# Kernel optimization log

Measured on AMD Instinct MI355X. Metric: run time of the kernel, lower is better.

Reference implementation:

```python
import jax, jax.numpy as jnp
import numpy as np

H = 8          # num_heads
BM = 128       # block_size_m
BN = 128       # block_size_n
EPS = 1e-6
CAUSAL = True  # config.causal


def setup_inputs() -> dict:
    key = jax.random.key(0)
    ks = jax.random.split(key, 5)
    B, N, D = 1, 2048, 512
    s = 1.0 / np.sqrt(D)
    # small-scale x so projected points mostly stay inside the Poincare ball
    x = jax.random.normal(ks[0], (B, N, D), jnp.float32) * 0.05
    return {
        'x': x,
        'c': jnp.ones((1,), jnp.float32),
        'Wq': jax.random.normal(ks[1], (D, D), jnp.float32) * s,
        'bq': jnp.zeros((D,), jnp.float32),
        'Wk': jax.random.normal(ks[2], (D, D), jnp.float32) * s,
        'bk': jnp.zeros((D,), jnp.float32),
        'Wv': jax.random.normal(ks[3], (D, D), jnp.float32) * s,
        'bv': jnp.zeros((D,), jnp.float32),
        'Wo': jax.random.normal(ks[4], (D, D), jnp.float32) * s,
        'bo': jnp.zeros((D,), jnp.float32),
    }


def reference(x, c, Wq, bq, Wk, bk, Wv, bv, Wo, bo):
    B, N, D = x.shape
    Dh = D // H
    cc = jnp.clip(jnp.abs(c), 1e-6)            # (1,) learned curvature, abs+clamp as in torch
    sqrt_c = jnp.sqrt(jnp.clip(cc, EPS))

    def proj(W, b):
        return (x @ W + b).reshape(B, N, H, Dh).transpose(0, 2, 1, 3)  # (B,H,N,Dh)

    q, k, v = proj(Wq, bq), proj(Wk, bk), proj(Wv, bv)

    # Poincare distance: ||q-k||^2 expanded via norms (same math as explicit diff tensor)
    qn = (q ** 2).sum(-1)                      # (B,H,N)
    kn = (k ** 2).sum(-1)                      # (B,H,N)
    qk = jnp.einsum('bhmd,bhnd->bhmn', q, k)   # (B,H,N,N)
    diff_sq = jnp.clip(qn[..., :, None] + kn[..., None, :] - 2.0 * qk, 0.0)
    denom = jnp.clip((1.0 - cc * qn)[..., :, None] * (1.0 - cc * kn)[..., None, :], EPS)
    arg = jnp.clip(1.0 + 2.0 * cc * diff_sq / denom, 1.0 + EPS)
    scores = -jnp.arccosh(arg) / sqrt_c        # (B,H,N,N)

    # block-wise softmax: each 128x128 block subtracts ITS OWN max (faithful to torch code,
    # which omits cross-block max rescaling), then exp-sums are accumulated across blocks.
    nbm, nbn = N // BM, N // BN
    s = scores.reshape(B, H, nbm, BM, nbn, BN)
    row = jnp.arange(nbm)[:, None]
    col = jnp.arange(nbn)[None, :]
    skip = (col > row) if CAUSAL else jnp.zeros((nbm, nbn), bool)   # skipped upper blocks
    diag = (col == row) if CAUSAL else jnp.zeros((nbm, nbn), bool)
    tri = jnp.triu(jnp.ones((BM, BN), bool), 1)
    mask = skip[:, None, :, None] | (diag[:, None, :, None] & tri[None, :, None, :])  # (nbm,BM,nbn,BN)

    s_masked = jnp.where(mask, -jnp.inf, s)
    bmax = s_masked.max(axis=-1, keepdims=True)                      # per-block-row max over BN
    bmax = jnp.where(jnp.isfinite(bmax), bmax, 0.0)                  # skipped blocks -> safe
    e = jnp.where(mask, 0.0, jnp.exp(s - bmax))                      # (B,H,nbm,BM,nbn,BN)

    normalizer = jnp.clip(e.sum(axis=(4, 5)).reshape(B, H, N), EPS)  # (B,H,N)
    vb = v.reshape(B, H, nbn, BN, Dh)
    out = jnp.einsum('bhrmcn,bhcnd->bhrmd', e, vb).reshape(B, H, N, Dh)
    out = out / normalizer[..., None]
    out = out.transpose(0, 2, 1, 3).reshape(B, N, D)
    return out @ Wo + bo
```

## Files before the change

kernel.cpp:

```cpp
#include <hip/hip_runtime.h>
#include <math.h>

#define D_MODEL 512
#define NHEADS  8
#define NSEQ    2048
#define NBLK    16
#define NCHUNK  72
#define EPSF    1e-6f
#define WPLANE  262144

typedef _Float16 v8h __attribute__((ext_vector_type(8)));
typedef _Float16 v4h __attribute__((ext_vector_type(4)));
typedef float    v4f __attribute__((ext_vector_type(4)));

static __device__ __forceinline__ v4f mfma16h(v8h a, v8h b, v4f c) {
  return __builtin_amdgcn_mfma_f32_16x16x32_f16(a, b, c, 0, 0, 0);
}

__global__ __launch_bounds__(256) void prep_wx(const float* __restrict__ W0,
                                               const float* __restrict__ W1,
                                               const float* __restrict__ W2,
                                               const float* __restrict__ W3,
                                               const float* __restrict__ x,
                                               _Float16* __restrict__ Wth,
                                               _Float16* __restrict__ xh) {
  const int z = blockIdx.z;
  const int tid = threadIdx.x;
  if (z == 4) {
    const int wg = blockIdx.y * 8 + blockIdx.x;
    int base = wg * 4096 + tid;
#pragma unroll
    for (int l = 0; l < 16; ++l) {
      int idx = base + l * 256;
      float4 v = reinterpret_cast<const float4*>(x)[idx];
      v4h o;
      o[0] = (_Float16)v.x; o[1] = (_Float16)v.y;
      o[2] = (_Float16)v.z; o[3] = (_Float16)v.w;
      reinterpret_cast<v4h*>(xh)[idx] = o;
    }
    return;
  }
  __shared__ float T[64][68];
  const float* W = (z == 0) ? W0 : (z == 1) ? W1 : (z == 2) ? W2 : W3;
  const int kb = blockIdx.x * 64;
  const int nb = blockIdx.y * 64;
#pragma unroll
  for (int l = 0; l < 4; ++l) {
    int f = tid + l * 256;
    int row = f >> 4, c4 = f & 15;
    float4 v = *reinterpret_cast<const float4*>(&W[(size_t)(kb + row) * D_MODEL + nb + c4 * 4]);
    T[c4 * 4 + 0][row] = v.x; T[c4 * 4 + 1][row] = v.y;
    T[c4 * 4 + 2][row] = v.z; T[c4 * 4 + 3][row] = v.w;
  }
  __syncthreads();
  _Float16* oh = Wth + (size_t)z * WPLANE;
#pragma unroll
  for (int l = 0; l < 4; ++l) {
    int f = tid + l * 256;
    int n_ = f >> 4, k4 = f & 15;
    v4h h4;
    h4[0] = (_Float16)T[n_][k4 * 4 + 0];
    h4[1] = (_Float16)T[n_][k4 * 4 + 1];
    h4[2] = (_Float16)T[n_][k4 * 4 + 2];
    h4[3] = (_Float16)T[n_][k4 * 4 + 3];
    *reinterpret_cast<v4h*>(&oh[(size_t)(nb + n_) * D_MODEL + kb + k4 * 4]) = h4;
  }
}

__global__ __launch_bounds__(256) void qkv_gemm(
    const _Float16* __restrict__ xh, const _Float16* __restrict__ Wth,
    const float* __restrict__ bq, const float* __restrict__ bk,
    const float* __restrict__ bv,
    _Float16* __restrict__ Qp, _Float16* __restrict__ Kp,
    _Float16* __restrict__ Vtb,
    float* __restrict__ Qn_, float* __restrict__ Kn_) {
  __shared__ _Float16 Ah[64][72];
  __shared__ _Float16 Bh[64][72];
  __shared__ float npar[2][64];
  const int z = blockIdx.z;
  const _Float16* Bt = Wth + (size_t)z * WPLANE;
  const float* bias = (z == 0) ? bq : (z == 1) ? bk : bv;
  _Float16* outp = (z == 0) ? Qp : Kp;

  const int bx = blockIdx.x, by = blockIdx.y;
  const int tid = threadIdx.x;
  const int wid = tid >> 6, lane = tid & 63;
  const int wr = wid >> 1, wc = wid & 1;
  const int g = lane >> 4, lx = lane & 15;

  v4f acc[2][2];
#pragma unroll
  for (int i = 0; i < 2; ++i)
#pragma unroll
    for (int j = 0; j < 2; ++j) acc[i][j] = v4f{0.f, 0.f, 0.f, 0.f};

  for (int k0 = 0; k0 < 8; ++k0) {
    __syncthreads();
#pragma unroll
    for (int l = 0; l < 2; ++l) {
      int f = tid + l * 256;
      int row = f >> 3, c8 = f & 7;
      *reinterpret_cast<uint4*>(&Ah[row][c8 * 8]) =
          *reinterpret_cast<const uint4*>(&xh[(size_t)(by * 64 + row) * D_MODEL + k0 * 64 + c8 * 8]);
      *reinterpret_cast<uint4*>(&Bh[row][c8 * 8]) =
          *reinterpret_cast<const uint4*>(&Bt[(size_t)(bx * 64 + row) * D_MODEL + k0 * 64 + c8 * 8]);
    }
    __syncthreads();
    v8h a[2][2], b[2][2];
#pragma unroll
    for (int i = 0; i < 2; ++i)
#pragma unroll
      for (int ks = 0; ks < 2; ++ks) {
        a[i][ks] = *reinterpret_cast<const v8h*>(&Ah[wr * 32 + i * 16 + lx][ks * 32 + g * 8]);
        b[i][ks] = *reinterpret_cast<const v8h*>(&Bh[wc * 32 + i * 16 + lx][ks * 32 + g * 8]);
      }
#pragma unroll
    for (int i = 0; i < 2; ++i)
#pragma unroll
      for (int j = 0; j < 2; ++j) {
        acc[i][j] = mfma16h(a[i][0], b[j][0], acc[i][j]);
        acc[i][j] = mfma16h(a[i][1], b[j][1], acc[i][j]);
      }
  }

  if (z < 2) {
    float np[2][4];
#pragma unroll
    for (int i = 0; i < 2; ++i)
#pragma unroll
      for (int r = 0; r < 4; ++r) np[i][r] = 0.f;
#pragma unroll
    for (int j = 0; j < 2; ++j) {
      const int col = bx * 64 + wc * 32 + j * 16 + lx;
      const float bj = bias[col];
#pragma unroll
      for (int i = 0; i < 2; ++i)
#pragma unroll
        for (int r = 0; r < 4; ++r) {
          const int row = by * 64 + wr * 32 + i * 16 + g * 4 + r;
          float v = acc[i][j][r] + bj;
          _Float16 hv = (_Float16)v;
          outp[(size_t)row * D_MODEL + col] = hv;
          float vr = (float)hv;
          np[i][r] = fmaf(vr, vr, np[i][r]);
        }
    }
#pragma unroll
    for (int i = 0; i < 2; ++i)
#pragma unroll
      for (int r = 0; r < 4; ++r) {
        float s = np[i][r];
        s += __shfl_xor(s, 1, 64);
        s += __shfl_xor(s, 2, 64);
        s += __shfl_xor(s, 4, 64);
        s += __shfl_xor(s, 8, 64);
        if (lx == 0) npar[wc][wr * 32 + i * 16 + g * 4 + r] = s;
      }
    __syncthreads();
    if (tid < 64) {
      float s = npar[0][tid] + npar[1][tid];
      float* Nout = (z == 0) ? Qn_ : Kn_;
      Nout[bx * NSEQ + by * 64 + tid] = s;
    }
  } else {
    __syncthreads();
    _Float16* Tv = &Ah[0][0];
#pragma unroll
    for (int j = 0; j < 2; ++j) {
      const int col = wc * 32 + j * 16 + lx;
      const float bj = bias[bx * 64 + col];
#pragma unroll
      for (int i = 0; i < 2; ++i)
#pragma unroll
        for (int r = 0; r < 4; ++r) {
          const int row = wr * 32 + i * 16 + g * 4 + r;
          Tv[row * 72 + col] = (_Float16)(acc[i][j][r] + bj);
        }
    }
    __syncthreads();
#pragma unroll
    for (int l = 0; l < 2; ++l) {
      int f = tid + l * 256;
      int d = f >> 3, ch = f & 7;
      ushort tmp[8];
#pragma unroll
      for (int jj = 0; jj < 8; ++jj)
        tmp[jj] = ((const ushort*)Tv)[(ch * 8 + jj) * 72 + d];
      *reinterpret_cast<uint4*>(&Vtb[(size_t)(bx * 64 + d) * NSEQ + by * 64 + ch * 8]) =
          *reinterpret_cast<const uint4*>(tmp);
    }
  }
}

__global__ __launch_bounds__(512, 4) void attn(
    const _Float16* __restrict__ Qp, const _Float16* __restrict__ Kp,
    const _Float16* __restrict__ Vtb, const float* __restrict__ Qn,
    const float* __restrict__ Kn, const float* __restrict__ cptr,
    _Float16* __restrict__ Opart, float* __restrict__ Npart)
{
  __shared__ _Float16 Khs[128][68];
  __shared__ _Float16 Vs[64][140];
  __shared__ _Float16 Es[8][16][68];
  __shared__ float kns[128];

  const int bid = blockIdx.x;
  const int h    = bid & 7;
  const int pid2 = bid >> 3;
  int m = 0, base = 0;
  while (base + (m / 2 + 1) <= pid2) { base += m / 2 + 1; ++m; }
  const int c  = pid2 - base;
  const int n0 = 2 * c;
  const int n1 = (n0 + 1 < m) ? n0 + 1 : m;

  const int tid  = threadIdx.x;
  const int w    = tid >> 6;
  const int lane = tid & 63;
  const int g = lane >> 4, lx = lane & 15;

  const float cc = fmaxf(fabsf(cptr[0]), 1e-6f);
  const float is = rsqrtf(cc);
  const bool is_one = (cc == 1.0f);
  const float two_cc = 2.f * cc;

  const int krow = tid >> 3, kc8 = tid & 7;
  const int vrow = tid >> 4, vc8 = tid & 15;

  const _Float16* Kgh = Kp + h * 64;
  const _Float16* Vgh = Vtb + (size_t)(h * 64) * NSEQ;

  {
    const _Float16* Kg = Kgh + (size_t)(n0 * 128) * D_MODEL;
    uint4 k0v = *reinterpret_cast<const uint4*>(&Kg[(size_t)krow * D_MODEL + kc8 * 8]);
    uint4 k1v = *reinterpret_cast<const uint4*>(&Kg[(size_t)(krow + 64) * D_MODEL + kc8 * 8]);
    uint4 v0v = *reinterpret_cast<const uint4*>(&Vgh[(size_t)vrow * NSEQ + n0 * 128 + vc8 * 8]);
    uint4 v1v = *reinterpret_cast<const uint4*>(&Vgh[(size_t)(vrow + 32) * NSEQ + n0 * 128 + vc8 * 8]);
    *reinterpret_cast<uint4*>(&Khs[krow][kc8 * 8]) = k0v;
    *reinterpret_cast<uint4*>(&Khs[krow + 64][kc8 * 8]) = k1v;
    *reinterpret_cast<uint4*>(&Vs[vrow][vc8 * 8]) = v0v;
    *reinterpret_cast<uint4*>(&Vs[vrow + 32][vc8 * 8]) = v1v;
    if (tid < 128) kns[tid] = Kn[h * NSEQ + n0 * 128 + tid];
  }
  __syncthreads();

  v8h aQ[2];
  {
    const size_t qoff = (size_t)(m * 128 + 16 * w + lx) * D_MODEL + h * 64 + g * 8;
    aQ[0] = *reinterpret_cast<const v8h*>(&Qp[qoff]);
    aQ[1] = *reinterpret_cast<const v8h*>(&Qp[qoff + 32]);
  }
  float qnr[4], qar[4];
#pragma unroll
  for (int r = 0; r < 4; ++r) {
    qnr[r] = Qn[h * NSEQ + m * 128 + 16 * w + g * 4 + r];
    qar[r] = fmaf(-cc, qnr[r], 1.f);
  }

  v4f o_acc[4];
#pragma unroll
  for (int td = 0; td < 4; ++td) o_acc[td] = v4f{0.f, 0.f, 0.f, 0.f};
  float nrm[4] = {0.f, 0.f, 0.f, 0.f};

  for (int n = n0; n <= n1; ++n) {
    v4f acc[8];
#pragma unroll
    for (int tn = 0; tn < 8; ++tn) {
      v8h b0 = *reinterpret_cast<const v8h*>(&Khs[tn * 16 + lx][g * 8]);
      v8h b1 = *reinterpret_cast<const v8h*>(&Khs[tn * 16 + lx][g * 8 + 32]);
      v4f a = v4f{0.f, 0.f, 0.f, 0.f};
      a = mfma16h(aQ[0], b0, a);
      a = mfma16h(aQ[1], b1, a);
      acc[tn] = a;
    }

    const bool diag = (n == m);
#pragma unroll
    for (int tn = 0; tn < 8; ++tn) {
      const int col = tn * 16 + lx;
      const float knc = kns[col];
      const float kac = fmaf(-cc, knc, 1.f);
#pragma unroll
      for (int r = 0; r < 4; ++r) {
        const int rowl = 16 * w + g * 4 + r;
        float dsq = fmaxf(fmaf(-2.f, acc[tn][r], qnr[r] + knc), 0.f);
        float den = fmaxf(qar[r] * kac, EPSF);
        float t = fmaxf(two_cc * dsq * __builtin_amdgcn_rcpf(den), EPSF);
        float u = 1.f + t + __builtin_amdgcn_sqrtf(t * (t + 2.f));
        if (diag && col > rowl) u = __builtin_inff();
        acc[tn][r] = u;
      }
    }

    float mred[4];
    if (is_one) {
#pragma unroll
      for (int r = 0; r < 4; ++r) mred[r] = __builtin_inff();
#pragma unroll
      for (int tn = 0; tn < 8; ++tn)
#pragma unroll
        for (int r = 0; r < 4; ++r) mred[r] = fminf(mred[r], acc[tn][r]);
#pragma unroll
      for (int d = 1; d < 16; d <<= 1)
#pragma unroll
        for (int r = 0; r < 4; ++r) mred[r] = fminf(mred[r], __shfl_xor(mred[r], d, 64));
    } else {
#pragma unroll
      for (int r = 0; r < 4; ++r) mred[r] = -__builtin_inff();
#pragma unroll
      for (int tn = 0; tn < 8; ++tn)
#pragma unroll
        for (int r = 0; r < 4; ++r) {
          float s = -__logf(acc[tn][r]) * is;
          acc[tn][r] = s;
          mred[r] = fmaxf(mred[r], s);
        }
#pragma unroll
      for (int d = 1; d < 16; d <<= 1)
#pragma unroll
        for (int r = 0; r < 4; ++r) mred[r] = fmaxf(mred[r], __shfl_xor(mred[r], d, 64));
    }

#pragma unroll
    for (int half = 0; half < 2; ++half) {
#pragma unroll
      for (int tn2 = 0; tn2 < 4; ++tn2) {
        const int tn = half * 4 + tn2;
#pragma unroll
        for (int r = 0; r < 4; ++r) {
          float e = is_one ? mred[r] * __builtin_amdgcn_rcpf(acc[tn][r])
                           : __expf(acc[tn][r] - mred[r]);
          nrm[r] += e;
          Es[w][g * 4 + r][tn2 * 16 + lx] = (_Float16)e;
        }
      }
      asm volatile("s_waitcnt lgkmcnt(0)" ::: "memory");
      __builtin_amdgcn_sched_barrier(0);
#pragma unroll
      for (int ks2 = 0; ks2 < 2; ++ks2) {
        const int ks = half * 2 + ks2;
        v8h ea = *reinterpret_cast<const v8h*>(&Es[w][lx][ks2 * 32 + g * 8]);
#pragma unroll
        for (int td = 0; td < 4; ++td) {
          v8h vb = *reinterpret_cast<const v8h*>(&Vs[td * 16 + lx][ks * 32 + g * 8]);
          o_acc[td] = mfma16h(ea, vb, o_acc[td]);
        }
      }
    }

    if (n < n1) {
      __syncthreads();
      const _Float16* Kg = Kgh + (size_t)((n + 1) * 128) * D_MODEL;
      uint4 k0v = *reinterpret_cast<const uint4*>(&Kg[(size_t)krow * D_MODEL + kc8 * 8]);
      uint4 k1v = *reinterpret_cast<const uint4*>(&Kg[(size_t)(krow + 64) * D_MODEL + kc8 * 8]);
      uint4 v0v = *reinterpret_cast<const uint4*>(&Vgh[(size_t)vrow * NSEQ + (n + 1) * 128 + vc8 * 8]);
      uint4 v1v = *reinterpret_cast<const uint4*>(&Vgh[(size_t)(vrow + 32) * NSEQ + (n + 1) * 128 + vc8 * 8]);
      *reinterpret_cast<uint4*>(&Khs[krow][kc8 * 8]) = k0v;
      *reinterpret_cast<uint4*>(&Khs[krow + 64][kc8 * 8]) = k1v;
      *reinterpret_cast<uint4*>(&Vs[vrow][vc8 * 8]) = v0v;
      *reinterpret_cast<uint4*>(&Vs[vrow + 32][vc8 * 8]) = v1v;
      if (tid < 128) kns[tid] = Kn[h * NSEQ + (n + 1) * 128 + tid];
      __syncthreads();
    }
  }

#pragma unroll
  for (int d = 1; d < 16; d <<= 1)
#pragma unroll
    for (int r = 0; r < 4; ++r) nrm[r] += __shfl_xor(nrm[r], d, 64);

  _Float16* Op = Opart + ((size_t)h * NCHUNK + pid2) * 8192;
#pragma unroll
  for (int td = 0; td < 4; ++td)
#pragma unroll
    for (int r = 0; r < 4; ++r)
      Op[(size_t)(((w * 4 + td) * 4) + r) * 64 + lane] = (_Float16)o_acc[td][r];

  {
    const int sel = lane & 3;
    float tmp = (sel == 0) ? nrm[0] : (sel == 1) ? nrm[1] : (sel == 2) ? nrm[2] : nrm[3];
    const int src = ((lane >> 2) & 3) * 16 + (lane & 3);
    float nval = __shfl(tmp, src, 64);
    if (lane < 16)
      Npart[((size_t)h * NCHUNK + pid2) * 128 + 16 * w + lane] = nval;
  }
}

__global__ __launch_bounds__(256) void reduce_o(const _Float16* __restrict__ Opart,
                                                const float* __restrict__ Npart,
                                                _Float16* __restrict__ Of) {
  const int mq = blockIdx.x;
  const int mm = mq >> 2;
  const int rq = (mq & 3) * 32;
  const int h  = blockIdx.y;
  const int tid = threadIdx.x;
  int base = 0;
  for (int k = 0; k < mm; ++k) base += k / 2 + 1;
  const int nch = mm / 2 + 1;

  __shared__ float T[32][68];
  __shared__ float innorm[32];
  if (tid < 32) {
    float s = 0.f;
    for (int cI = 0; cI < nch; ++cI)
      s += Npart[((size_t)h * NCHUNK + base + cI) * 128 + rq + tid];
    innorm[tid] = 1.f / fmaxf(s, EPSF);
  }
  const int wbase = rq >> 4;
#pragma unroll
  for (int l = 0; l < 8; ++l) {
    int idx = tid + l * 256;
    int lane = idx & 63;
    int sub  = idx >> 6;
    int r = sub & 3, td = (sub >> 2) & 3, wloc = sub >> 4;
    int w = wbase + wloc;
    const size_t off = (size_t)((w * 4 + td) * 4 + r) * 64 + lane;
    float s = 0.f;
    for (int cI = 0; cI < nch; ++cI)
      s += (float)Opart[((size_t)h * NCHUNK + base + cI) * 8192 + off];
    int row = 16 * wloc + 4 * (lane >> 4) + r;
    int col = td * 16 + (lane & 15);
    T[row][col] = s;
  }
  __syncthreads();
#pragma unroll
  for (int l = 0; l < 2; ++l) {
    int f = tid + l * 256;
    int row = f >> 4, c4 = f & 15;
    float inv = innorm[row];
    v4h o4;
    o4[0] = (_Float16)(T[row][c4 * 4 + 0] * inv);
    o4[1] = (_Float16)(T[row][c4 * 4 + 1] * inv);
    o4[2] = (_Float16)(T[row][c4 * 4 + 2] * inv);
    o4[3] = (_Float16)(T[row][c4 * 4 + 3] * inv);
    *reinterpret_cast<v4h*>(
        &Of[(size_t)(mm * 128 + rq + row) * D_MODEL + h * 64 + c4 * 4]) = o4;
  }
}

__global__ __launch_bounds__(256) void o_gemm(const _Float16* __restrict__ Of,
                                              const _Float16* __restrict__ Wth,
                                              const float* __restrict__ bo,
                                              float* __restrict__ out) {
  __shared__ _Float16 As[64][40], Bs[64][40];
  const _Float16* Bt = Wth + (size_t)3 * WPLANE;
  const int bx = blockIdx.x, by = blockIdx.y;
  const int tid = threadIdx.x;
  const int wid = tid >> 6, lane = tid & 63;
  const int wr = wid >> 1, wc = wid & 1;
  const int g = lane >> 4, lx = lane & 15;

  v4f acc[2][2];
#pragma unroll
  for (int i = 0; i < 2; ++i)
#pragma unroll
    for (int j = 0; j < 2; ++j) acc[i][j] = v4f{0.f, 0.f, 0.f, 0.f};

  const int srow = tid >> 2, sc8 = tid & 3;
  for (int k0 = 0; k0 < 16; ++k0) {
    __syncthreads();
    *reinterpret_cast<uint4*>(&As[srow][sc8 * 8]) =
        *reinterpret_cast<const uint4*>(&Of[(size_t)(by * 64 + srow) * D_MODEL + k0 * 32 + sc8 * 8]);
    *reinterpret_cast<uint4*>(&Bs[srow][sc8 * 8]) =
        *reinterpret_cast<const uint4*>(&Bt[(size_t)(bx * 64 + srow) * D_MODEL + k0 * 32 + sc8 * 8]);
    __syncthreads();
    v8h ah[2], bh[2];
#pragma unroll
    for (int i = 0; i < 2; ++i) {
      ah[i] = *reinterpret_cast<const v8h*>(&As[wr * 32 + i * 16 + lx][g * 8]);
      bh[i] = *reinterpret_cast<const v8h*>(&Bs[wc * 32 + i * 16 + lx][g * 8]);
    }
#pragma unroll
    for (int i = 0; i < 2; ++i)
#pragma unroll
      for (int j = 0; j < 2; ++j)
        acc[i][j] = mfma16h(ah[i], bh[j], acc[i][j]);
  }
#pragma unroll
  for (int j = 0; j < 2; ++j) {
    const int col = bx * 64 + wc * 32 + j * 16 + lx;
    const float bj = bo[col];
#pragma unroll
    for (int i = 0; i < 2; ++i)
#pragma unroll
      for (int r = 0; r < 4; ++r) {
        const int row = by * 64 + wr * 32 + i * 16 + g * 4 + r;
        out[(size_t)row * D_MODEL + col] = acc[i][j][r] + bj;
      }
  }
}

extern "C" void kernel_launch(void* const* d_in, const int* in_sizes, int n_in,
                              void* d_out, int out_size, void* d_ws, size_t ws_size,
                              hipStream_t stream) {
  (void)in_sizes; (void)n_in; (void)out_size; (void)ws_size;
  const float* x  = (const float*)d_in[0];
  const float* cfg= (const float*)d_in[1];
  const float* Wq = (const float*)d_in[2];
  const float* bq = (const float*)d_in[3];
  const float* Wk = (const float*)d_in[4];
  const float* bk = (const float*)d_in[5];
  const float* Wv = (const float*)d_in[6];
  const float* bv = (const float*)d_in[7];
  const float* Wo = (const float*)d_in[8];
  const float* bo = (const float*)d_in[9];
  float* out = (float*)d_out;

  char* p = (char*)d_ws;
  const size_t PL = (size_t)NSEQ * D_MODEL * sizeof(_Float16);
  _Float16* Wth = (_Float16*)p;        p += 4 * (size_t)WPLANE * sizeof(_Float16);
  _Float16* xhp = (_Float16*)p;        p += PL;
  _Float16* Qp  = (_Float16*)p;        p += PL;
  _Float16* Kp  = (_Float16*)p;        p += PL;
  _Float16* Vtb = (_Float16*)p;        p += PL;
  _Float16* Of  = (_Float16*)p;        p += PL;
  float*  Qn  = (float*)p;             p += (size_t)NHEADS * NSEQ * sizeof(float);
  float*  Kn  = (float*)p;             p += (size_t)NHEADS * NSEQ * sizeof(float);
  _Float16* Opart = (_Float16*)p;      p += (size_t)NHEADS * NCHUNK * 8192 * sizeof(_Float16);
  float*  Npart = (float*)p;

  prep_wx<<<dim3(8, 8, 5), 256, 0, stream>>>(Wq, Wk, Wv, Wo, x, Wth, xhp);
  qkv_gemm<<<dim3(8, 32, 3), 256, 0, stream>>>(xhp, Wth, bq, bk, bv,
                                               Qp, Kp, Vtb, Qn, Kn);
  attn<<<dim3(NCHUNK * NHEADS), 512, 0, stream>>>(Qp, Kp, Vtb, Qn, Kn, cfg,
                                                  Opart, Npart);
  reduce_o<<<dim3(64, NHEADS), 256, 0, stream>>>(Opart, Npart, Of);
  o_gemm<<<dim3(8, 32), 256, 0, stream>>>(Of, Wth, bo, out);
}
```

Baseline: 79.67 us.

## Load K/V tiles via direct global-to-LDS with XOR swizzle and overlap

Replaces register-staged K/V tile loads with global_load_lds direct-to-shared transfers into XOR-swizzled unpadded LDS layouts. The next block's K is issued right after the current QK MFMAs, and its V after the current PV pass, so the loads overlap with the softmax and PV work. Both blocks' key norms are loaded up front. This removes the VGPR round trip and one barrier per iteration, at the cost of relying on manual vmcnt waits and the hardware's lane-to-LDS mapping for correctness.

```diff
diff --git a/kernel.cpp b/kernel.cpp
--- a/kernel.cpp
+++ b/kernel.cpp
@@ -16,6 +16,11 @@
 static __device__ __forceinline__ v4f mfma16h(v8h a, v8h b, v4f c) {
   return __builtin_amdgcn_mfma_f32_16x16x32_f16(a, b, c, 0, 0, 0);
 }
+
+#define GLLDS(gp, lp)                                                          \
+  __builtin_amdgcn_global_load_lds(                                            \
+      (const __attribute__((address_space(1))) unsigned int*)(const void*)(gp),\
+      (__attribute__((address_space(3))) unsigned int*)(void*)(lp), 16, 0, 0)
 
 __global__ __launch_bounds__(256) void prep_wx(const float* __restrict__ W0,
                                                const float* __restrict__ W1,
@@ -198,10 +203,10 @@
     const float* __restrict__ Kn, const float* __restrict__ cptr,
     _Float16* __restrict__ Opart, float* __restrict__ Npart)
 {
-  __shared__ _Float16 Khs[128][68];
-  __shared__ _Float16 Vs[64][140];
+  __shared__ _Float16 KhsF[8192];
+  __shared__ _Float16 VsF[8192];
   __shared__ _Float16 Es[8][16][68];
-  __shared__ float kns[128];
+  __shared__ float kns2[256];
 
   const int bid = blockIdx.x;
   const int h    = bid & 7;
@@ -211,6 +216,7 @@
   const int c  = pid2 - base;
   const int n0 = 2 * c;
   const int n1 = (n0 + 1 < m) ? n0 + 1 : m;
+  const bool two = (n1 != n0);
 
   const int tid  = threadIdx.x;
   const int w    = tid >> 6;
@@ -222,25 +228,33 @@
   const bool is_one = (cc == 1.0f);
   const float two_cc = 2.f * cc;
 
-  const int krow = tid >> 3, kc8 = tid & 7;
-  const int vrow = tid >> 4, vc8 = tid & 15;
-
   const _Float16* Kgh = Kp + h * 64;
   const _Float16* Vgh = Vtb + (size_t)(h * 64) * NSEQ;
 
-  {
-    const _Float16* Kg = Kgh + (size_t)(n0 * 128) * D_MODEL;
-    uint4 k0v = *reinterpret_cast<const uint4*>(&Kg[(size_t)krow * D_MODEL + kc8 * 8]);
-    uint4 k1v = *reinterpret_cast<const uint4*>(&Kg[(size_t)(krow + 64) * D_MODEL + kc8 * 8]);
-    uint4 v0v = *reinterpret_cast<const uint4*>(&Vgh[(size_t)vrow * NSEQ + n0 * 128 + vc8 * 8]);
-    uint4 v1v = *reinterpret_cast<const uint4*>(&Vgh[(size_t)(vrow + 32) * NSEQ + n0 * 128 + vc8 * 8]);
-    *reinterpret_cast<uint4*>(&Khs[krow][kc8 * 8]) = k0v;
-    *reinterpret_cast<uint4*>(&Khs[krow + 64][kc8 * 8]) = k1v;
-    *reinterpret_cast<uint4*>(&Vs[vrow][vc8 * 8]) = v0v;
-    *reinterpret_cast<uint4*>(&Vs[vrow + 32][vc8 * 8]) = v1v;
-    if (tid < 128) kns[tid] = Kn[h * NSEQ + n0 * 128 + tid];
-  }
-  __syncthreads();
+  const int krow0 = tid >> 3;
+  const int klc   = (tid & 7) ^ (krow0 & 7);
+  const int vd0   = tid >> 4;
+  const int vlc   = (tid & 15) ^ (vd0 & 7);
+
+#define ISSUE_K(nn)                                                           \
+  do {                                                                        \
+    GLLDS(&Kgh[(size_t)((nn) * 128 + krow0) * D_MODEL + klc * 8],             \
+          &KhsF[w * 512]);                                                    \
+    GLLDS(&Kgh[(size_t)((nn) * 128 + krow0 + 64) * D_MODEL + klc * 8],        \
+          &KhsF[4096 + w * 512]);                                             \
+  } while (0)
+#define ISSUE_V(nn)                                                           \
+  do {                                                                        \
+    GLLDS(&Vgh[(size_t)vd0 * NSEQ + (nn) * 128 + vlc * 8],                    \
+          &VsF[w * 512]);                                                     \
+    GLLDS(&Vgh[(size_t)(vd0 + 32) * NSEQ + (nn) * 128 + vlc * 8],             \
+          &VsF[4096 + w * 512]);                                              \
+  } while (0)
+
+  ISSUE_K(n0);
+  ISSUE_V(n0);
+  if (tid < 128) kns2[tid] = Kn[h * NSEQ + n0 * 128 + tid];
+  else if (two && tid < 256) kns2[tid] = Kn[h * NSEQ + n1 * 128 + (tid - 128)];
 
   v8h aQ[2];
   {
@@ -260,23 +274,50 @@
   for (int td = 0; td < 4; ++td) o_acc[td] = v4f{0.f, 0.f, 0.f, 0.f};
   float nrm[4] = {0.f, 0.f, 0.f, 0.f};
 
-  for (int n = n0; n <= n1; ++n) {
-    v4f acc[8];
-#pragma unroll
-    for (int tn = 0; tn < 8; ++tn) {
-      v8h b0 = *reinterpret_cast<const v8h*>(&Khs[tn * 16 + lx][g * 8]);
-      v8h b1 = *reinterpret_cast<const v8h*>(&Khs[tn * 16 + lx][g * 8 + 32]);
-      v4f a = v4f{0.f, 0.f, 0.f, 0.f};
-      a = mfma16h(aQ[0], b0, a);
-      a = mfma16h(aQ[1], b1, a);
-      acc[tn] = a;
+  __syncthreads();
+
+  v4f acc[8];
+  const int swz = lx & 7;
+
+#pragma unroll
+  for (int tn = 0; tn < 8; ++tn) {
+    const int rb = (tn * 16 + lx) * 64;
+    v8h b0 = *reinterpret_cast<const v8h*>(&KhsF[rb + ((g ^ swz) * 8)]);
+    v8h b1 = *reinterpret_cast<const v8h*>(&KhsF[rb + (((g ^ swz) ^ 4) * 8)]);
+    v4f a = v4f{0.f, 0.f, 0.f, 0.f};
+    a = mfma16h(aQ[0], b0, a);
+    a = mfma16h(aQ[1], b1, a);
+    acc[tn] = a;
+  }
+  if (two) {
+    __syncthreads();
+    ISSUE_K(n1);
+  }
+
+#pragma unroll
+  for (int it = 0; it < 2; ++it) {
+    if (it == 1 && !two) break;
+    const int n = (it == 0) ? n0 : n1;
+    const int kofs = it * 128;
+
+    if (it == 1) {
+#pragma unroll
+      for (int tn = 0; tn < 8; ++tn) {
+        const int rb = (tn * 16 + lx) * 64;
+        v8h b0 = *reinterpret_cast<const v8h*>(&KhsF[rb + ((g ^ swz) * 8)]);
+        v8h b1 = *reinterpret_cast<const v8h*>(&KhsF[rb + (((g ^ swz) ^ 4) * 8)]);
+        v4f a = v4f{0.f, 0.f, 0.f, 0.f};
+        a = mfma16h(aQ[0], b0, a);
+        a = mfma16h(aQ[1], b1, a);
+        acc[tn] = a;
+      }
     }
 
     const bool diag = (n == m);
 #pragma unroll
     for (int tn = 0; tn < 8; ++tn) {
       const int col = tn * 16 + lx;
-      const float knc = kns[col];
+      const float knc = kns2[kofs + col];
       const float kac = fmaf(-cc, knc, 1.f);
 #pragma unroll
       for (int r = 0; r < 4; ++r) {
@@ -332,7 +373,11 @@
           Es[w][g * 4 + r][tn2 * 16 + lx] = (_Float16)e;
         }
       }
-      asm volatile("s_waitcnt lgkmcnt(0)" ::: "memory");
+      if (it == 1 && half == 0) {
+        asm volatile("s_waitcnt vmcnt(0) lgkmcnt(0)" ::: "memory");
+      } else {
+        asm volatile("s_waitcnt lgkmcnt(0)" ::: "memory");
+      }
       __builtin_amdgcn_sched_barrier(0);
 #pragma unroll
       for (int ks2 = 0; ks2 < 2; ++ks2) {
@@ -340,25 +385,16 @@
         v8h ea = *reinterpret_cast<const v8h*>(&Es[w][lx][ks2 * 32 + g * 8]);
 #pragma unroll
         for (int td = 0; td < 4; ++td) {
-          v8h vb = *reinterpret_cast<const v8h*>(&Vs[td * 16 + lx][ks * 32 + g * 8]);
+          v8h vb = *reinterpret_cast<const v8h*>(
+              &VsF[(td * 16 + lx) * 128 + (((ks * 4 + g) ^ swz) * 8)]);
           o_acc[td] = mfma16h(ea, vb, o_acc[td]);
         }
       }
     }
 
-    if (n < n1) {
+    if (it == 0 && two) {
       __syncthreads();
-      const _Float16* Kg = Kgh + (size_t)((n + 1) * 128) * D_MODEL;
-      uint4 k0v = *reinterpret_cast<const uint4*>(&Kg[(size_t)krow * D_MODEL + kc8 * 8]);
-      uint4 k1v = *reinterpret_cast<const uint4*>(&Kg[(size_t)(krow + 64) * D_MODEL + kc8 * 8]);
-      uint4 v0v = *reinterpret_cast<const uint4*>(&Vgh[(size_t)vrow * NSEQ + (n + 1) * 128 + vc8 * 8]);
-      uint4 v1v = *reinterpret_cast<const uint4*>(&Vgh[(size_t)(vrow + 32) * NSEQ + (n + 1) * 128 + vc8 * 8]);
-      *reinterpret_cast<uint4*>(&Khs[krow][kc8 * 8]) = k0v;
-      *reinterpret_cast<uint4*>(&Khs[krow + 64][kc8 * 8]) = k1v;
-      *reinterpret_cast<uint4*>(&Vs[vrow][vc8 * 8]) = v0v;
-      *reinterpret_cast<uint4*>(&Vs[vrow + 32][vc8 * 8]) = v1v;
-      if (tid < 128) kns[tid] = Kn[h * NSEQ + (n + 1) * 128 + tid];
-      __syncthreads();
+      ISSUE_V(n1);
     }
   }
 
@@ -382,6 +418,8 @@
     if (lane < 16)
       Npart[((size_t)h * NCHUNK + pid2) * 128 + 16 * w + lane] = nval;
   }
+#undef ISSUE_K
+#undef ISSUE_V
 }
 
 __global__ __launch_bounds__(256) void reduce_o(const _Float16* __restrict__ Opart,
```

After: 78.37 us (median of 2 runs). No clear change (-1.6%).
